# Kernel tuning notes

Hardware: AMD Instinct MI355X
Metric: run time of the kernel (lower is better)

The kernel has to match this reference:

```python
import jax, jax.numpy as jnp
import numpy as np

C_CURV = 1.0          # manifold curvature c
MIN_NORM = 1e-15      # hgcn min-norm clamp
ATANH_EPS = 1e-6      # artanh arg clamp (fp32-safe version of hgcn's 1e-15)

N_NODES, DIM, N_EDGES, N_CLASSES = 100000, 128, 1000000, 4


def setup_inputs() -> dict:
    key = jax.random.key(0)
    k1, k2, k3 = jax.random.split(key, 3)
    x = jax.random.normal(k1, (N_NODES, DIM), dtype=jnp.float32)
    idx = jax.random.randint(k2, (N_EDGES, 2), 0, N_NODES, dtype=jnp.int64)
    W = jax.random.normal(k3, (2 * DIM, N_CLASSES), dtype=jnp.float32) * 0.05
    b = jnp.zeros((N_CLASSES,), dtype=jnp.float32)
    return {"x": x, "idx": idx, "W": W, "b": b}


def _logmap0(x, c):
    # PoincareBall.logmap0: scale = artanh(sqrt(c)*||x||) / (sqrt(c)*||x||)
    sqrt_c = c ** 0.5
    norm = jnp.maximum(jnp.linalg.norm(x, axis=-1, keepdims=True), MIN_NORM)
    a = jnp.clip(sqrt_c * norm, -1.0 + ATANH_EPS, 1.0 - ATANH_EPS)
    return (jnp.arctanh(a) / (sqrt_c * norm)) * x


def reference(x, idx, W, b):
    # proj_tan0 is identity for the Poincare ball
    h = _logmap0(x, C_CURV)                                   # [N, D]
    edge_feat = jnp.concatenate([h[idx[:, 0]], h[idx[:, 1]]], axis=1)  # [E, 2D]
    # Linear with identity activation (dropout=0 at inference)
    return edge_feat @ W + b                                  # [E, n_classes]
```

## Files before the change

kernel.cpp:

```cpp
#include <hip/hip_runtime.h>
#include <hip/hip_bf16.h>


#define DIM 128

typedef float f32x4 __attribute__((ext_vector_type(4)));
typedef int   i32x2 __attribute__((ext_vector_type(2)));

__global__ __launch_bounds__(256) void node_proj_kernel(
    const float* __restrict__ x, const float* __restrict__ W,
    const float* __restrict__ b, float* __restrict__ y, int n_nodes)
{
    __shared__ float wp[1152];
    const int t = threadIdx.x;
    {
        const int r = t & 127, h = t >> 7;
        const f32x4 wv = ((const f32x4*)W)[t];
        *(f32x4*)(wp + r * 8 + (r >> 2) * 4 + h * 4) = wv;
    }
    __syncthreads();

    const int lane = t & 63;
    const int li   = lane & 3;
    const int gid  = lane >> 2;
    const int wid  = blockIdx.x * (blockDim.x >> 6) + (t >> 6);
    const int n0   = wid * 16 + gid;
    if (n0 >= n_nodes) return;

    const f32x4* xp0 = (const f32x4*)(x + (size_t)n0 * DIM + li * 4);
    const float* wl  = wp + li * 36;

    float acc[9];
#pragma unroll
    for (int i = 0; i < 9; ++i) acc[i] = 0.f;

#pragma unroll
    for (int j = 0; j < 8; ++j) {
        const f32x4 a4 = xp0[j * 4];
#pragma unroll
        for (int k = 0; k < 4; ++k) {
            const f32x4 wa = *(const f32x4*)(wl + j * 144 + k * 8);
            const f32x4 wb = *(const f32x4*)(wl + j * 144 + k * 8 + 4);
            const float a = a4[k];
            acc[0] += a * a;
            acc[1] += a * wa[0];
            acc[2] += a * wa[1];
            acc[3] += a * wa[2];
            acc[4] += a * wa[3];
            acc[5] += a * wb[0];
            acc[6] += a * wb[1];
            acc[7] += a * wb[2];
            acc[8] += a * wb[3];
        }
    }

#pragma unroll
    for (int i = 0; i < 9; ++i) {
        acc[i] += __shfl_xor(acc[i], 1, 64);
        acc[i] += __shfl_xor(acc[i], 2, 64);
    }

    if (li < 2) {
        const bool second = li;

        float norm = fmaxf(sqrtf(acc[0]), 1e-15f);
        const float aa  = fminf(norm, 1.0f - 1e-6f);
        const float art = 0.5f * log1pf(2.0f * aa / (1.0f - aa));
        const float scale = art / norm;

        const float w0 = second ? acc[5] : acc[1];
        const float w1 = second ? acc[6] : acc[2];
        const float w2 = second ? acc[7] : acc[3];
        const float w3 = second ? acc[8] : acc[4];

        const f32x4 bv4 = *(const f32x4*)b;
        f32x4 o;
        o[0] = w0 * scale + (second ? 0.f : bv4[0]);
        o[1] = w1 * scale + (second ? 0.f : bv4[1]);
        o[2] = w2 * scale + (second ? 0.f : bv4[2]);
        o[3] = w3 * scale + (second ? 0.f : bv4[3]);

        *(f32x4*)(y + (size_t)n0 * 8 + li * 4) = o;
    }
}

__global__ __launch_bounds__(256) void edge_kernel(
    const int* __restrict__ idx, const float* __restrict__ y,
    float* __restrict__ out, int n_edges)
{
    const int e = blockIdx.x * blockDim.x + threadIdx.x;
    if (e >= n_edges) return;
    const i32x2 ii = __builtin_nontemporal_load((const i32x2*)idx + e);
    const f32x4 a0 = *(const f32x4*)(y + (size_t)ii[0] * 8);
    const f32x4 c0 = *(const f32x4*)(y + (size_t)ii[1] * 8 + 4);
    const f32x4 o0 = a0 + c0;
    __builtin_nontemporal_store(o0, (f32x4*)out + e);
}

extern "C" void kernel_launch(void* const* d_in, const int* in_sizes, int n_in,
                              void* d_out, int out_size, void* d_ws, size_t ws_size,
                              hipStream_t stream) {
    const float* x   = (const float*)d_in[0];
    const int*   idx = (const int*)d_in[1];
    const float* W   = (const float*)d_in[2];
    const float* b   = (const float*)d_in[3];
    float* out = (float*)d_out;

    const int n_nodes = in_sizes[0] / DIM;
    const int n_edges = in_sizes[1] / 2;

    float* y = (float*)d_ws;

    const int blocks1 = (n_nodes + 63) / 64;
    node_proj_kernel<<<blocks1, 256, 0, stream>>>(x, W, b, y, n_nodes);

    const int blocks2 = (n_edges + 255) / 256;
    edge_kernel<<<blocks2, 256, 0, stream>>>(idx, y, out, n_edges);
}
```

Baseline: 30.55 us.

## Compute node projection with one thread per node and scalar-loaded weights

Restructures the node projection kernel so each thread processes a whole node row, instead of four lanes per node combined by shuffle reductions. The weight matrix is no longer staged in LDS; it is read directly from global memory at wave-uniform addresses, so it can be served by scalar loads. Row loads are double-buffered in registers to keep more memory requests in flight. The trade-off is far fewer waves in total, worse per-instruction coalescing across lanes, and higher register pressure.

Result: slower. 32.58 us (+6.6%).

```diff
diff --git a/kernel.cpp b/kernel.cpp
--- a/kernel.cpp
+++ b/kernel.cpp
@@ -7,81 +7,69 @@
 typedef float f32x4 __attribute__((ext_vector_type(4)));
 typedef int   i32x2 __attribute__((ext_vector_type(2)));
 
-__global__ __launch_bounds__(256) void node_proj_kernel(
+__global__ __launch_bounds__(64) void node_proj_kernel(
     const float* __restrict__ x, const float* __restrict__ W,
     const float* __restrict__ b, float* __restrict__ y, int n_nodes)
 {
-    __shared__ float wp[1152];
-    const int t = threadIdx.x;
-    {
-        const int r = t & 127, h = t >> 7;
-        const f32x4 wv = ((const f32x4*)W)[t];
-        *(f32x4*)(wp + r * 8 + (r >> 2) * 4 + h * 4) = wv;
-    }
-    __syncthreads();
+    const int n = blockIdx.x * 64 + threadIdx.x;
+    if (n >= n_nodes) return;
 
-    const int lane = t & 63;
-    const int li   = lane & 3;
-    const int gid  = lane >> 2;
-    const int wid  = blockIdx.x * (blockDim.x >> 6) + (t >> 6);
-    const int n0   = wid * 16 + gid;
-    if (n0 >= n_nodes) return;
-
-    const f32x4* xp0 = (const f32x4*)(x + (size_t)n0 * DIM + li * 4);
-    const float* wl  = wp + li * 36;
+    const f32x4* xp = (const f32x4*)(x + (size_t)n * DIM);
 
     float acc[9];
 #pragma unroll
     for (int i = 0; i < 9; ++i) acc[i] = 0.f;
 
+    f32x4 cur[8], nxt[8];
 #pragma unroll
-    for (int j = 0; j < 8; ++j) {
-        const f32x4 a4 = xp0[j * 4];
+    for (int q = 0; q < 8; ++q) cur[q] = xp[q];
+
 #pragma unroll
-        for (int k = 0; k < 4; ++k) {
-            const f32x4 wa = *(const f32x4*)(wl + j * 144 + k * 8);
-            const f32x4 wb = *(const f32x4*)(wl + j * 144 + k * 8 + 4);
-            const float a = a4[k];
-            acc[0] += a * a;
-            acc[1] += a * wa[0];
-            acc[2] += a * wa[1];
-            acc[3] += a * wa[2];
-            acc[4] += a * wa[3];
-            acc[5] += a * wb[0];
-            acc[6] += a * wb[1];
-            acc[7] += a * wb[2];
-            acc[8] += a * wb[3];
+    for (int c = 0; c < 4; ++c) {
+        if (c < 3) {
+#pragma unroll
+            for (int q = 0; q < 8; ++q) nxt[q] = xp[(c + 1) * 8 + q];
         }
+#pragma unroll
+        for (int q = 0; q < 8; ++q) {
+#pragma unroll
+            for (int k = 0; k < 4; ++k) {
+                const int d = c * 32 + q * 4 + k;
+                const float a = cur[q][k];
+                const float* Wd = W + 4 * d;
+                acc[0] = fmaf(a, a, acc[0]);
+                acc[1] = fmaf(a, Wd[0], acc[1]);
+                acc[2] = fmaf(a, Wd[1], acc[2]);
+                acc[3] = fmaf(a, Wd[2], acc[3]);
+                acc[4] = fmaf(a, Wd[3], acc[4]);
+                acc[5] = fmaf(a, Wd[512], acc[5]);
+                acc[6] = fmaf(a, Wd[513], acc[6]);
+                acc[7] = fmaf(a, Wd[514], acc[7]);
+                acc[8] = fmaf(a, Wd[515], acc[8]);
+            }
+        }
+#pragma unroll
+        for (int q = 0; q < 8; ++q) cur[q] = nxt[q];
     }
 
-#pragma unroll
-    for (int i = 0; i < 9; ++i) {
-        acc[i] += __shfl_xor(acc[i], 1, 64);
-        acc[i] += __shfl_xor(acc[i], 2, 64);
-    }
+    float norm = fmaxf(sqrtf(acc[0]), 1e-15f);
+    const float aa  = fminf(norm, 1.0f - 1e-6f);
+    const float art = 0.5f * log1pf(2.0f * aa / (1.0f - aa));
+    const float scale = art / norm;
 
-    if (li < 2) {
-        const bool second = li;
+    f32x4 o0, o1;
+    o0[0] = fmaf(acc[1], scale, b[0]);
+    o0[1] = fmaf(acc[2], scale, b[1]);
+    o0[2] = fmaf(acc[3], scale, b[2]);
+    o0[3] = fmaf(acc[4], scale, b[3]);
+    o1[0] = acc[5] * scale;
+    o1[1] = acc[6] * scale;
+    o1[2] = acc[7] * scale;
+    o1[3] = acc[8] * scale;
 
-        float norm = fmaxf(sqrtf(acc[0]), 1e-15f);
-        const float aa  = fminf(norm, 1.0f - 1e-6f);
-        const float art = 0.5f * log1pf(2.0f * aa / (1.0f - aa));
-        const float scale = art / norm;
-
-        const float w0 = second ? acc[5] : acc[1];
-        const float w1 = second ? acc[6] : acc[2];
-        const float w2 = second ? acc[7] : acc[3];
-        const float w3 = second ? acc[8] : acc[4];
-
-        const f32x4 bv4 = *(const f32x4*)b;
-        f32x4 o;
-        o[0] = w0 * scale + (second ? 0.f : bv4[0]);
-        o[1] = w1 * scale + (second ? 0.f : bv4[1]);
-        o[2] = w2 * scale + (second ? 0.f : bv4[2]);
-        o[3] = w3 * scale + (second ? 0.f : bv4[3]);
-
-        *(f32x4*)(y + (size_t)n0 * 8 + li * 4) = o;
-    }
+    f32x4* yp = (f32x4*)(y + (size_t)n * 8);
+    yp[0] = o0;
+    yp[1] = o1;
 }
 
 __global__ __launch_bounds__(256) void edge_kernel(
@@ -112,7 +100,7 @@
     float* y = (float*)d_ws;
 
     const int blocks1 = (n_nodes + 63) / 64;
-    node_proj_kernel<<<blocks1, 256, 0, stream>>>(x, W, b, y, n_nodes);
+    node_proj_kernel<<<blocks1, 64, 0, stream>>>(x, W, b, y, n_nodes);
 
     const int blocks2 = (n_edges + 255) / 256;
     edge_kernel<<<blocks2, 256, 0, stream>>>(idx, y, out, n_edges);
```

## Use 8 lanes per node with contiguous 64B row chunks in node projection

Applied to the files above, without the earlier changes.

The node projection kernel now assigns 8 lanes per node instead of 4, each lane loading a contiguous 16-float slice of the row up front. The shared weight layout is re-padded to match, and an extra shuffle stage is added to the reduction. This halves nodes per block and doubles the block count, aiming for more memory parallelism and more independent loads in flight when streaming x. The cost is a third shuffle round and fewer nodes per lane, and the new per-lane row slices may coalesce differently than the old interleaved access.

Measured after the change: 31.46 us. 3.0% more time.

```diff
diff --git a/kernel.cpp b/kernel.cpp
--- a/kernel.cpp
+++ b/kernel.cpp
@@ -11,46 +11,49 @@
     const float* __restrict__ x, const float* __restrict__ W,
     const float* __restrict__ b, float* __restrict__ y, int n_nodes)
 {
-    __shared__ float wp[1152];
+    __shared__ float wp[1056];
     const int t = threadIdx.x;
     {
+        const f32x4 wv = ((const f32x4*)W)[t];
         const int r = t & 127, h = t >> 7;
-        const f32x4 wv = ((const f32x4*)W)[t];
-        *(f32x4*)(wp + r * 8 + (r >> 2) * 4 + h * 4) = wv;
+        *(f32x4*)(wp + r * 8 + (r >> 4) * 4 + h * 4) = wv;
     }
     __syncthreads();
 
     const int lane = t & 63;
-    const int li   = lane & 3;
-    const int gid  = lane >> 2;
-    const int wid  = blockIdx.x * (blockDim.x >> 6) + (t >> 6);
-    const int n0   = wid * 16 + gid;
-    if (n0 >= n_nodes) return;
+    const int li   = lane & 7;
+    const int g    = lane >> 3;
+    const int n    = blockIdx.x * 32 + (t >> 6) * 8 + g;
+    if (n >= n_nodes) return;
 
-    const f32x4* xp0 = (const f32x4*)(x + (size_t)n0 * DIM + li * 4);
-    const float* wl  = wp + li * 36;
+    const f32x4* xp = (const f32x4*)(x + (size_t)n * DIM + li * 16);
+    const float* wl = wp + li * 132;
+
+    f32x4 xa[4];
+#pragma unroll
+    for (int q = 0; q < 4; ++q) xa[q] = xp[q];
 
     float acc[9];
 #pragma unroll
     for (int i = 0; i < 9; ++i) acc[i] = 0.f;
 
 #pragma unroll
-    for (int j = 0; j < 8; ++j) {
-        const f32x4 a4 = xp0[j * 4];
+    for (int q = 0; q < 4; ++q) {
 #pragma unroll
         for (int k = 0; k < 4; ++k) {
-            const f32x4 wa = *(const f32x4*)(wl + j * 144 + k * 8);
-            const f32x4 wb = *(const f32x4*)(wl + j * 144 + k * 8 + 4);
-            const float a = a4[k];
-            acc[0] += a * a;
-            acc[1] += a * wa[0];
-            acc[2] += a * wa[1];
-            acc[3] += a * wa[2];
-            acc[4] += a * wa[3];
-            acc[5] += a * wb[0];
-            acc[6] += a * wb[1];
-            acc[7] += a * wb[2];
-            acc[8] += a * wb[3];
+            const int idx = q * 4 + k;
+            const f32x4 wa = *(const f32x4*)(wl + idx * 8);
+            const f32x4 wb = *(const f32x4*)(wl + idx * 8 + 4);
+            const float a = xa[q][k];
+            acc[0] = fmaf(a, a, acc[0]);
+            acc[1] = fmaf(a, wa[0], acc[1]);
+            acc[2] = fmaf(a, wa[1], acc[2]);
+            acc[3] = fmaf(a, wa[2], acc[3]);
+            acc[4] = fmaf(a, wa[3], acc[4]);
+            acc[5] = fmaf(a, wb[0], acc[5]);
+            acc[6] = fmaf(a, wb[1], acc[6]);
+            acc[7] = fmaf(a, wb[2], acc[7]);
+            acc[8] = fmaf(a, wb[3], acc[8]);
         }
     }
 
@@ -58,6 +61,7 @@
     for (int i = 0; i < 9; ++i) {
         acc[i] += __shfl_xor(acc[i], 1, 64);
         acc[i] += __shfl_xor(acc[i], 2, 64);
+        acc[i] += __shfl_xor(acc[i], 4, 64);
     }
 
     if (li < 2) {
@@ -75,12 +79,12 @@
 
         const f32x4 bv4 = *(const f32x4*)b;
         f32x4 o;
-        o[0] = w0 * scale + (second ? 0.f : bv4[0]);
-        o[1] = w1 * scale + (second ? 0.f : bv4[1]);
-        o[2] = w2 * scale + (second ? 0.f : bv4[2]);
-        o[3] = w3 * scale + (second ? 0.f : bv4[3]);
+        o[0] = fmaf(w0, scale, second ? 0.f : bv4[0]);
+        o[1] = fmaf(w1, scale, second ? 0.f : bv4[1]);
+        o[2] = fmaf(w2, scale, second ? 0.f : bv4[2]);
+        o[3] = fmaf(w3, scale, second ? 0.f : bv4[3]);
 
-        *(f32x4*)(y + (size_t)n0 * 8 + li * 4) = o;
+        *(f32x4*)(y + (size_t)n * 8 + li * 4) = o;
     }
 }
 
@@ -111,7 +115,7 @@
 
     float* y = (float*)d_ws;
 
-    const int blocks1 = (n_nodes + 63) / 64;
+    const int blocks1 = (n_nodes + 31) / 32;
     node_proj_kernel<<<blocks1, 256, 0, stream>>>(x, W, b, y, n_nodes);
 
     const int blocks2 = (n_edges + 255) / 256;
```
